# Optimization experiments

Hardware: AMD Instinct MI355X
Metric: run time of the kernel (lower is better)

The kernel has to match this reference:

```python
import jax, jax.numpy as jnp
import numpy as np

N_NODES = 100000
N_EDGES = 600000
DIMS = [128, 64, 32, 2]


def gcn_conv(x, edge_index, W, b, n_nodes):
    """PyG GCNConv (eval mode): symmetric-normalized aggregation with self-loops.
    out = D^{-1/2} (A + I) D^{-1/2} (x W) + b
    """
    h = x @ W  # [N, out] -- transform first (cheaper when out < in)
    src = jnp.concatenate([edge_index[0], jnp.arange(n_nodes)])  # add self-loops
    dst = jnp.concatenate([edge_index[1], jnp.arange(n_nodes)])
    deg = jax.ops.segment_sum(jnp.ones_like(dst, dtype=h.dtype), dst,
                              num_segments=n_nodes)  # in-degree incl. self-loop
    dinv = jax.lax.rsqrt(deg)
    norm = dinv[src] * dinv[dst]  # [E+N]
    msg = norm[:, None] * h[src]  # gather + scale
    out = jax.ops.segment_sum(msg, dst, num_segments=n_nodes)  # scatter-add
    return out + b


def setup_inputs() -> dict:
    key = jax.random.key(0)
    ks = jax.random.split(key, 8)
    x = jax.random.normal(ks[0], (N_NODES, DIMS[0]), dtype=jnp.float32)
    edge_index = jax.random.randint(ks[1], (2, N_EDGES), 0, N_NODES, dtype=jnp.int64)
    inp = {"x": x, "edge_index": edge_index}
    for i in range(3):
        fan_in, fan_out = DIMS[i], DIMS[i + 1]
        s = 1.0 / np.sqrt(fan_in)
        inp[f"W{i+1}"] = jax.random.uniform(ks[2 + 2 * i], (fan_in, fan_out),
                                            minval=-s, maxval=s, dtype=jnp.float32)
        inp[f"b{i+1}"] = jnp.zeros((fan_out,), dtype=jnp.float32)
    return inp


def reference(x, edge_index, W1, b1, W2, b2, W3, b3):
    # 3 stacked GCNConv layers with ReLU; dropout is identity in eval mode.
    n = x.shape[0]
    x = jax.nn.relu(gcn_conv(x, edge_index, W1, b1, n))
    x = jax.nn.relu(gcn_conv(x, edge_index, W2, b2, n))
    x = jax.nn.relu(gcn_conv(x, edge_index, W3, b3, n))
    return x
```

## Files before the change

### kernel.cpp

```cpp
#include <hip/hip_runtime.h>
#include <math.h>


#define FULL_GRID 2048
#define PARTS 8

typedef const __attribute__((address_space(1))) void* gas_ptr;
typedef __attribute__((address_space(3))) void* las_ptr;

__device__ __forceinline__ void gld16(const void* g, void* l) {
  __builtin_amdgcn_global_load_lds((gas_ptr)g, (las_ptr)l, 16, 0, 0);
}

__global__ __launch_bounds__(256) void k_zero(int* __restrict__ p, int n4) {
  int i = blockIdx.x * blockDim.x + threadIdx.x;
  const int stride = gridDim.x * blockDim.x;
  int4* p4 = (int4*)p;
  for (; i < n4; i += stride) p4[i] = make_int4(0, 0, 0, 0);
}

__global__ __launch_bounds__(256) void k_detect(const unsigned int* __restrict__ words,
                                                int* __restrict__ flag) {
  __shared__ int sm[256];
  int cnt = 0;
  #pragma unroll
  for (int j = 0; j < 8; ++j) {
    int idx = (threadIdx.x * 8 + j) * 2 + 1;
    cnt += (words[idx] == 0u) ? 1 : 0;
  }
  sm[threadIdx.x] = cnt;
  __syncthreads();
  for (int off = 128; off > 0; off >>= 1) {
    if (threadIdx.x < off) sm[threadIdx.x] += sm[threadIdx.x + off];
    __syncthreads();
  }
  if (threadIdx.x == 0) flag[0] = (sm[0] > 1024) ? 1 : 0;
}

__global__ __launch_bounds__(256) void k_hist(const void* __restrict__ eraw, int E,
                                              int N, const int* __restrict__ flag,
                                              int* __restrict__ counts) {
  const int is64 = flag[0];
  const int part = blockIdx.x & (PARTS - 1);
  const int lo = (int)((long long)N * part / PARTS);
  const int hi = (int)((long long)N * (part + 1) / PARTS);
  int i = (blockIdx.x >> 3) * blockDim.x + threadIdx.x;
  const int stride = (gridDim.x >> 3) * blockDim.x;
  if (is64) {
    const long long* e = (const long long*)eraw;
    for (; i < E; i += stride) {
      const int d = (int)e[(long long)E + i];
      if (d >= lo && d < hi) atomicAdd(&counts[d], 1);
    }
  } else {
    const int* e = (const int*)eraw;
    for (; i < E; i += stride) {
      const int d = e[E + i];
      if (d >= lo && d < hi) atomicAdd(&counts[d], 1);
    }
  }
}

__global__ __launch_bounds__(1024) void k_scan1(const int* __restrict__ counts,
                                                int* __restrict__ scanned,
                                                int* __restrict__ partials, int n) {
  __shared__ int sm[1024];
  const int i = blockIdx.x * 1024 + threadIdx.x;
  const int v = (i < n) ? counts[i] : 0;
  sm[threadIdx.x] = v;
  __syncthreads();
  for (int off = 1; off < 1024; off <<= 1) {
    int t = sm[threadIdx.x];
    int u = (threadIdx.x >= off) ? sm[threadIdx.x - off] : 0;
    __syncthreads();
    sm[threadIdx.x] = t + u;
    __syncthreads();
  }
  const int inc = sm[threadIdx.x];
  if (i < n) scanned[i] = inc - v;
  if (threadIdx.x == 1023) partials[blockIdx.x] = inc;
}

__global__ __launch_bounds__(1024) void k_scan2(int* __restrict__ partials, int nb) {
  __shared__ int sm[1024];
  const int v = (threadIdx.x < nb) ? partials[threadIdx.x] : 0;
  sm[threadIdx.x] = v;
  __syncthreads();
  for (int off = 1; off < 1024; off <<= 1) {
    int t = sm[threadIdx.x];
    int u = (threadIdx.x >= off) ? sm[threadIdx.x - off] : 0;
    __syncthreads();
    sm[threadIdx.x] = t + u;
    __syncthreads();
  }
  if (threadIdx.x < nb) partials[threadIdx.x] = sm[threadIdx.x] - v;
}

__global__ __launch_bounds__(256) void k_scan3(const int* __restrict__ scanned,
                                               const int* __restrict__ partials,
                                               const int* __restrict__ counts,
                                               int* __restrict__ offsets,
                                               int* __restrict__ cursor,
                                               float* __restrict__ dinv, int n) {
  int i = blockIdx.x * blockDim.x + threadIdx.x;
  const int stride = gridDim.x * blockDim.x;
  for (; i < n; i += stride) {
    const int o = scanned[i] + partials[i >> 10];
    offsets[i] = o;
    cursor[i] = o;
    dinv[i] = rsqrtf((float)counts[i] + 1.0f);
  }
}

__global__ __launch_bounds__(256) void k_fill(const void* __restrict__ eraw, int E,
                                              int N, const int* __restrict__ flag,
                                              int* __restrict__ cursor,
                                              int* __restrict__ elist) {
  const int is64 = flag[0];
  const int part = blockIdx.x & (PARTS - 1);
  const int lo = (int)((long long)N * part / PARTS);
  const int hi = (int)((long long)N * (part + 1) / PARTS);
  int i = (blockIdx.x >> 3) * blockDim.x + threadIdx.x;
  const int stride = (gridDim.x >> 3) * blockDim.x;
  if (is64) {
    const long long* e = (const long long*)eraw;
    for (; i < E; i += stride) {
      const int d = (int)e[(long long)E + i];
      if (d >= lo && d < hi) {
        const int s = (int)e[i];
        elist[atomicAdd(&cursor[d], 1)] = s;
      }
    }
  } else {
    const int* e = (const int*)eraw;
    for (; i < E; i += stride) {
      const int d = e[E + i];
      if (d >= lo && d < hi) {
        const int s = e[i];
        elist[atomicAdd(&cursor[d], 1)] = s;
      }
    }
  }
}

template <int F_IN, int F_OUT, int TILE_M, int KC, int THREADS>
__global__ __launch_bounds__(THREADS) void k_transform(const float* __restrict__ X,
                                                       const float* __restrict__ W,
                                                       const float* __restrict__ dinv,
                                                       float* __restrict__ H, int n) {
  constexpr int COLT = F_OUT / 4;
  constexpr int ROWT = THREADS / COLT;
  constexpr int TM = TILE_M / ROWT;
  constexpr int NKC = F_IN / KC;
  constexpr int K4 = F_IN / 4;
  constexpr int NWB = (NKC > 1) ? 2 : 1;
  static_assert(TM * ROWT == TILE_M && COLT * 4 == F_OUT, "tiling");
  static_assert((TILE_M * F_IN * 4) % 1024 == 0 && (KC * F_OUT * 4) % 1024 == 0, "segs");
  static_assert(K4 >= 8, "swizzle range");
  static_assert(ROWT % 8 == 0, "swizzle invariance across r");

  __shared__ __align__(16) float Xs[TILE_M * F_IN];
  __shared__ __align__(16) float Ws[NWB][KC * F_OUT];

  const int tid = threadIdx.x;
  const int lane = tid & 63;
  const int wid = tid >> 6;
  constexpr int NWAVES = THREADS / 64;
  const long long base = (long long)blockIdx.x * TILE_M;

  const float4* __restrict__ X4 = (const float4*)X;
  if (base + TILE_M <= n) {
    constexpr int SEGS = TILE_M * F_IN * 4 / 1024;
    constexpr int PW = SEGS / NWAVES;
    #pragma unroll
    for (int j = 0; j < PW; ++j) {
      const int seg = wid * PW + j;
      const int slot = seg * 64 + lane;
      const int row = slot / K4;
      const int c = slot % K4;
      const int ksrc = c ^ (row & 7);
      gld16(&X4[(base + row) * K4 + ksrc], &Xs[seg * 256]);
    }
  } else {
    for (int slot = tid; slot < TILE_M * K4; slot += THREADS) {
      const int row = slot / K4;
      const int c = slot % K4;
      float4 v = make_float4(0.f, 0.f, 0.f, 0.f);
      if (base + row < n) v = X4[(base + row) * K4 + (c ^ (row & 7))];
      ((float4*)Xs)[slot] = v;
    }
  }

  constexpr int WSEG = KC * F_OUT * 4 / 1024;
  constexpr int WPW = WSEG / NWAVES;
  static_assert(WPW >= 1, "W seg per wave");
  {
    #pragma unroll
    for (int j = 0; j < WPW; ++j) {
      const int seg = wid * WPW + j;
      gld16(W + seg * 256 + lane * 4, &Ws[0][seg * 256]);
    }
  }

  const int ct = tid % COLT;
  const int rt = tid / COLT;
  const int sw = rt & 7;

  float4 acc[TM];
  #pragma unroll
  for (int r = 0; r < TM; ++r) acc[r] = make_float4(0.f, 0.f, 0.f, 0.f);

  const float4* Xs4 = (const float4*)Xs;

  for (int kc = 0; kc < NKC; ++kc) {
    __syncthreads();
    if (NKC > 1 && kc + 1 < NKC) {
      const float* wb = W + (kc + 1) * KC * F_OUT;
      #pragma unroll
      for (int j = 0; j < WPW; ++j) {
        const int seg = wid * WPW + j;
        gld16(wb + seg * 256 + lane * 4, &Ws[(kc + 1) & (NWB - 1)][seg * 256]);
      }
    }
    const float4* Ws4 = (const float4*)Ws[kc & (NWB - 1)];
    #pragma unroll
    for (int k4 = 0; k4 < KC / 4; ++k4) {
      const int kk = kc * (KC / 4) + k4;
      float4 wv0 = Ws4[(k4 * 4 + 0) * COLT + ct];
      float4 wv1 = Ws4[(k4 * 4 + 1) * COLT + ct];
      float4 wv2 = Ws4[(k4 * 4 + 2) * COLT + ct];
      float4 wv3 = Ws4[(k4 * 4 + 3) * COLT + ct];
      #pragma unroll
      for (int r = 0; r < TM; ++r) {
        const float4 xv = Xs4[(rt + r * ROWT) * K4 + (kk ^ sw)];
        acc[r].x = fmaf(xv.x, wv0.x, acc[r].x);
        acc[r].y = fmaf(xv.x, wv0.y, acc[r].y);
        acc[r].z = fmaf(xv.x, wv0.z, acc[r].z);
        acc[r].w = fmaf(xv.x, wv0.w, acc[r].w);
        acc[r].x = fmaf(xv.y, wv1.x, acc[r].x);
        acc[r].y = fmaf(xv.y, wv1.y, acc[r].y);
        acc[r].z = fmaf(xv.y, wv1.z, acc[r].z);
        acc[r].w = fmaf(xv.y, wv1.w, acc[r].w);
        acc[r].x = fmaf(xv.z, wv2.x, acc[r].x);
        acc[r].y = fmaf(xv.z, wv2.y, acc[r].y);
        acc[r].z = fmaf(xv.z, wv2.z, acc[r].z);
        acc[r].w = fmaf(xv.z, wv2.w, acc[r].w);
        acc[r].x = fmaf(xv.w, wv3.x, acc[r].x);
        acc[r].y = fmaf(xv.w, wv3.y, acc[r].y);
        acc[r].z = fmaf(xv.w, wv3.z, acc[r].z);
        acc[r].w = fmaf(xv.w, wv3.w, acc[r].w);
      }
    }
  }

  #pragma unroll
  for (int r = 0; r < TM; ++r) {
    const long long row = base + rt + r * ROWT;
    if (row < n) {
      const float di = dinv[row];
      float4 v = acc[r];
      v.x *= di; v.y *= di; v.z *= di; v.w *= di;
      *(float4*)&H[row * F_OUT + ct * 4] = v;
    }
  }
}

template <int F, bool RELU_OUT, bool FUSE_W3>
__global__ __launch_bounds__(256) void k_aggregate(const float* __restrict__ HS,
                                                   const float* __restrict__ dinv,
                                                   const int* __restrict__ offsets,
                                                   const int* __restrict__ counts,
                                                   const int* __restrict__ elist,
                                                   const float* __restrict__ bias,
                                                   const float* __restrict__ W3,
                                                   float* __restrict__ out, int n) {
  const int f = threadIdx.x % F;
  const int grp = threadIdx.x / F;
  constexpr int GRPS = 256 / F;
  const float bf = bias[f];
  float w30 = 0.f, w31 = 0.f;
  if (FUSE_W3) { w30 = W3[f * 2 + 0]; w31 = W3[f * 2 + 1]; }

  for (long long d = (long long)blockIdx.x * GRPS + grp; d < n;
       d += (long long)gridDim.x * GRPS) {
    const float di = dinv[d];
    float acc = HS[d * F + f];
    const int start = offsets[d];
    const int cnt = counts[d];
    for (int j = 0; j < cnt; j += 8) {
      int idx[8];
      float v[8];
      #pragma unroll
      for (int t = 0; t < 8; ++t) {
        const int jj = (j + t < cnt) ? (j + t) : j;
        idx[t] = elist[start + jj];
      }
      #pragma unroll
      for (int t = 0; t < 8; ++t) v[t] = HS[(long long)idx[t] * F + f];
      #pragma unroll
      for (int t = 0; t < 8; ++t) acc += (j + t < cnt) ? v[t] : 0.f;
    }

    float r = fmaf(di, acc, bf);
    if (RELU_OUT) r = fmaxf(r, 0.f);
    if (!FUSE_W3) {
      out[d * F + f] = r;
    } else {
      float t0 = r * w30, t1 = r * w31;
      #pragma unroll
      for (int m = 1; m < 32; m <<= 1) {
        t0 += __shfl_xor(t0, m, 64);
        t1 += __shfl_xor(t1, m, 64);
      }
      if (f == 0) {
        out[d * 2 + 0] = di * t0;
        out[d * 2 + 1] = di * t1;
      }
    }
  }
}

extern "C" void kernel_launch(void* const* d_in, const int* in_sizes, int n_in,
                              void* d_out, int out_size, void* d_ws, size_t ws_size,
                              hipStream_t stream) {
  const float* x = (const float*)d_in[0];
  const void* eraw = d_in[1];
  const float* W1 = (const float*)d_in[2];
  const float* b1 = (const float*)d_in[3];
  const float* W2 = (const float*)d_in[4];
  const float* b2 = (const float*)d_in[5];
  const float* W3 = (const float*)d_in[6];
  const float* b3 = (const float*)d_in[7];
  float* out = (float*)d_out;

  const int N = in_sizes[0] / 128;
  const int E = in_sizes[1] / 2;

  char* ws = (char*)d_ws;
  size_t off = 0;
  auto alloc = [&](size_t bytes) -> char* {
    char* p = ws + off;
    off = (off + bytes + 255) & ~(size_t)255;
    return p;
  };
  int*   flag     = (int*)alloc(256);
  int*   counts   = (int*)alloc((size_t)N * 4 + 16);
  int*   scanned  = (int*)alloc((size_t)N * 4);
  int*   partials = (int*)alloc(1024 * 4);
  int*   offsets  = (int*)alloc((size_t)N * 4);
  int*   cursor   = (int*)alloc((size_t)N * 4);
  int*   elist    = (int*)alloc((size_t)E * 4);
  float* dinv     = (float*)alloc((size_t)N * 4);
  float* hbuf     = (float*)alloc((size_t)N * 64 * 4);
  float* obuf     = (float*)alloc((size_t)N * 64 * 4);
  float* h2buf    = (float*)alloc((size_t)N * 32 * 4);
  (void)ws_size; (void)n_in; (void)out_size;

  k_zero<<<128, 256, 0, stream>>>(counts, (N + 3) / 4);
  k_detect<<<1, 256, 0, stream>>>((const unsigned int*)eraw, flag);
  k_hist<<<FULL_GRID, 256, 0, stream>>>(eraw, E, N, flag, counts);
  const int NB = (N + 1023) >> 10;
  k_scan1<<<NB, 1024, 0, stream>>>(counts, scanned, partials, N);
  k_scan2<<<1, 1024, 0, stream>>>(partials, NB);
  k_scan3<<<(N + 255) / 256, 256, 0, stream>>>(scanned, partials, counts, offsets,
                                               cursor, dinv, N);
  k_fill<<<FULL_GRID, 256, 0, stream>>>(eraw, E, N, flag, cursor, elist);

  k_transform<128, 64, 128, 16, 256><<<(N + 127) / 128, 256, 0, stream>>>(
      x, W1, dinv, hbuf, N);
  k_aggregate<64, true, false><<<(N + 3) / 4, 256, 0, stream>>>(
      hbuf, dinv, offsets, counts, elist, b1, nullptr, obuf, N);

  k_transform<64, 32, 128, 64, 256><<<(N + 127) / 128, 256, 0, stream>>>(
      obuf, W2, dinv, h2buf, N);
  k_aggregate<32, true, true><<<(N + 7) / 8, 256, 0, stream>>>(
      h2buf, dinv, offsets, counts, elist, b2, W3, hbuf, N);

  k_aggregate<2, true, false><<<(N + 127) / 128, 256, 0, stream>>>(
      hbuf, dinv, offsets, counts, elist, b3, nullptr, out, N);
}
```

Baseline: 197.1 us.

## Vectorize aggregation per wave, merge init kernels, fold scan2, shrink transform tile

Adds a wave-per-node aggregation kernel in which lanes load float4 slices of several neighbours at once and combine them with cross-lane shuffles, replacing the thread-per-feature gather for layers 1 and 2. It also merges the zero and dtype-detect kernels into one launch and drops the second scan kernel by having every scan3 block redo the small partials scan serially in shared memory. The first transform uses a smaller row tile. These cut launch count and per-edge index-load overhead, in exchange for redundant serial scan work in every block and more shuffle reduction per node.

New measurement: 194.2 us. No clear change (-1.5%).

```diff
diff --git a/kernel.cpp b/kernel.cpp
--- a/kernel.cpp
+++ b/kernel.cpp
@@ -12,29 +12,30 @@
   __builtin_amdgcn_global_load_lds((gas_ptr)g, (las_ptr)l, 16, 0, 0);
 }
 
-__global__ __launch_bounds__(256) void k_zero(int* __restrict__ p, int n4) {
+__global__ __launch_bounds__(256) void k_init(int* __restrict__ p, int n4,
+                                              const unsigned int* __restrict__ words,
+                                              int* __restrict__ flag) {
+  if (blockIdx.x == gridDim.x - 1) {
+    __shared__ int sm[256];
+    int cnt = 0;
+    #pragma unroll
+    for (int j = 0; j < 8; ++j) {
+      int idx = (threadIdx.x * 8 + j) * 2 + 1;
+      cnt += (words[idx] == 0u) ? 1 : 0;
+    }
+    sm[threadIdx.x] = cnt;
+    __syncthreads();
+    for (int off = 128; off > 0; off >>= 1) {
+      if (threadIdx.x < off) sm[threadIdx.x] += sm[threadIdx.x + off];
+      __syncthreads();
+    }
+    if (threadIdx.x == 0) flag[0] = (sm[0] > 1024) ? 1 : 0;
+    return;
+  }
   int i = blockIdx.x * blockDim.x + threadIdx.x;
-  const int stride = gridDim.x * blockDim.x;
+  const int stride = (gridDim.x - 1) * blockDim.x;
   int4* p4 = (int4*)p;
   for (; i < n4; i += stride) p4[i] = make_int4(0, 0, 0, 0);
-}
-
-__global__ __launch_bounds__(256) void k_detect(const unsigned int* __restrict__ words,
-                                                int* __restrict__ flag) {
-  __shared__ int sm[256];
-  int cnt = 0;
-  #pragma unroll
-  for (int j = 0; j < 8; ++j) {
-    int idx = (threadIdx.x * 8 + j) * 2 + 1;
-    cnt += (words[idx] == 0u) ? 1 : 0;
-  }
-  sm[threadIdx.x] = cnt;
-  __syncthreads();
-  for (int off = 128; off > 0; off >>= 1) {
-    if (threadIdx.x < off) sm[threadIdx.x] += sm[threadIdx.x + off];
-    __syncthreads();
-  }
-  if (threadIdx.x == 0) flag[0] = (sm[0] > 1024) ? 1 : 0;
 }
 
 __global__ __launch_bounds__(256) void k_hist(const void* __restrict__ eraw, int E,
@@ -81,31 +82,25 @@
   if (threadIdx.x == 1023) partials[blockIdx.x] = inc;
 }
 
-__global__ __launch_bounds__(1024) void k_scan2(int* __restrict__ partials, int nb) {
-  __shared__ int sm[1024];
-  const int v = (threadIdx.x < nb) ? partials[threadIdx.x] : 0;
-  sm[threadIdx.x] = v;
-  __syncthreads();
-  for (int off = 1; off < 1024; off <<= 1) {
-    int t = sm[threadIdx.x];
-    int u = (threadIdx.x >= off) ? sm[threadIdx.x - off] : 0;
-    __syncthreads();
-    sm[threadIdx.x] = t + u;
-    __syncthreads();
-  }
-  if (threadIdx.x < nb) partials[threadIdx.x] = sm[threadIdx.x] - v;
-}
-
 __global__ __launch_bounds__(256) void k_scan3(const int* __restrict__ scanned,
                                                const int* __restrict__ partials,
+                                               int nb,
                                                const int* __restrict__ counts,
                                                int* __restrict__ offsets,
                                                int* __restrict__ cursor,
                                                float* __restrict__ dinv, int n) {
+  __shared__ int ps[1024];
+  for (int t = threadIdx.x; t < nb; t += 256) ps[t] = partials[t];
+  __syncthreads();
+  if (threadIdx.x == 0) {
+    int run = 0;
+    for (int b = 0; b < nb; ++b) { const int v = ps[b]; ps[b] = run; run += v; }
+  }
+  __syncthreads();
   int i = blockIdx.x * blockDim.x + threadIdx.x;
   const int stride = gridDim.x * blockDim.x;
   for (; i < n; i += stride) {
-    const int o = scanned[i] + partials[i >> 10];
+    const int o = scanned[i] + ps[i >> 10];
     offsets[i] = o;
     cursor[i] = o;
     dinv[i] = rsqrtf((float)counts[i] + 1.0f);
@@ -143,13 +138,13 @@
   }
 }
 
-template <int F_IN, int F_OUT, int TILE_M, int KC, int THREADS>
-__global__ __launch_bounds__(THREADS) void k_transform(const float* __restrict__ X,
-                                                       const float* __restrict__ W,
-                                                       const float* __restrict__ dinv,
-                                                       float* __restrict__ H, int n) {
+template <int F_IN, int F_OUT, int TILE_M, int KC>
+__global__ __launch_bounds__(256) void k_transform(const float* __restrict__ X,
+                                                   const float* __restrict__ W,
+                                                   const float* __restrict__ dinv,
+                                                   float* __restrict__ H, int n) {
   constexpr int COLT = F_OUT / 4;
-  constexpr int ROWT = THREADS / COLT;
+  constexpr int ROWT = 256 / COLT;
   constexpr int TM = TILE_M / ROWT;
   constexpr int NKC = F_IN / KC;
   constexpr int K4 = F_IN / 4;
@@ -165,13 +160,12 @@
   const int tid = threadIdx.x;
   const int lane = tid & 63;
   const int wid = tid >> 6;
-  constexpr int NWAVES = THREADS / 64;
   const long long base = (long long)blockIdx.x * TILE_M;
 
   const float4* __restrict__ X4 = (const float4*)X;
   if (base + TILE_M <= n) {
     constexpr int SEGS = TILE_M * F_IN * 4 / 1024;
-    constexpr int PW = SEGS / NWAVES;
+    constexpr int PW = SEGS / 4;
     #pragma unroll
     for (int j = 0; j < PW; ++j) {
       const int seg = wid * PW + j;
@@ -182,7 +176,7 @@
       gld16(&X4[(base + row) * K4 + ksrc], &Xs[seg * 256]);
     }
   } else {
-    for (int slot = tid; slot < TILE_M * K4; slot += THREADS) {
+    for (int slot = tid; slot < TILE_M * K4; slot += 256) {
       const int row = slot / K4;
       const int c = slot % K4;
       float4 v = make_float4(0.f, 0.f, 0.f, 0.f);
@@ -192,8 +186,7 @@
   }
 
   constexpr int WSEG = KC * F_OUT * 4 / 1024;
-  constexpr int WPW = WSEG / NWAVES;
-  static_assert(WPW >= 1, "W seg per wave");
+  constexpr int WPW = WSEG / 4;
   {
     #pragma unroll
     for (int j = 0; j < WPW; ++j) {
@@ -266,20 +259,99 @@
 }
 
 template <int F, bool RELU_OUT, bool FUSE_W3>
+__global__ __launch_bounds__(256) void k_agg_vec(const float* __restrict__ HS,
+                                                 const float* __restrict__ dinv,
+                                                 const int* __restrict__ offsets,
+                                                 const int* __restrict__ counts,
+                                                 const int* __restrict__ elist,
+                                                 const float* __restrict__ bias,
+                                                 const float* __restrict__ W3,
+                                                 float* __restrict__ out, int n) {
+  constexpr int LPE = F / 4;
+  constexpr int EPW = 64 / LPE;
+  const int lane = threadIdx.x & 63;
+  const int wv = (blockIdx.x * (blockDim.x >> 6)) + (threadIdx.x >> 6);
+  const int nwaves = gridDim.x * (blockDim.x >> 6);
+  const int g = lane / LPE;
+  const int fl = lane % LPE;
+  const float4 bf = *(const float4*)&bias[fl * 4];
+
+  float w3a0 = 0.f, w3a1 = 0.f, w3a2 = 0.f, w3a3 = 0.f;
+  float w3b0 = 0.f, w3b1 = 0.f, w3b2 = 0.f, w3b3 = 0.f;
+  if (FUSE_W3) {
+    w3a0 = W3[(fl * 4 + 0) * 2 + 0]; w3b0 = W3[(fl * 4 + 0) * 2 + 1];
+    w3a1 = W3[(fl * 4 + 1) * 2 + 0]; w3b1 = W3[(fl * 4 + 1) * 2 + 1];
+    w3a2 = W3[(fl * 4 + 2) * 2 + 0]; w3b2 = W3[(fl * 4 + 2) * 2 + 1];
+    w3a3 = W3[(fl * 4 + 3) * 2 + 0]; w3b3 = W3[(fl * 4 + 3) * 2 + 1];
+  }
+
+  for (long long d = wv; d < n; d += nwaves) {
+    const float di = dinv[d];
+    const int start = offsets[d];
+    const int cnt = counts[d];
+    float4 acc = make_float4(0.f, 0.f, 0.f, 0.f);
+    if (g == 0) acc = *(const float4*)&HS[d * F + fl * 4];
+
+    for (int j = 0; j < cnt; j += 2 * EPW) {
+      const int e0 = j + g;
+      const int e1 = j + EPW + g;
+      const int i0 = elist[start + (e0 < cnt ? e0 : cnt - 1)];
+      const int i1 = elist[start + (e1 < cnt ? e1 : cnt - 1)];
+      const float4 v0 = *(const float4*)&HS[(long long)i0 * F + fl * 4];
+      const float4 v1 = *(const float4*)&HS[(long long)i1 * F + fl * 4];
+      if (e0 < cnt) {
+        acc.x += v0.x; acc.y += v0.y; acc.z += v0.z; acc.w += v0.w;
+      }
+      if (e1 < cnt) {
+        acc.x += v1.x; acc.y += v1.y; acc.z += v1.z; acc.w += v1.w;
+      }
+    }
+    #pragma unroll
+    for (int m = LPE; m < 64; m <<= 1) {
+      acc.x += __shfl_xor(acc.x, m, 64);
+      acc.y += __shfl_xor(acc.y, m, 64);
+      acc.z += __shfl_xor(acc.z, m, 64);
+      acc.w += __shfl_xor(acc.w, m, 64);
+    }
+    float4 r;
+    r.x = fmaf(di, acc.x, bf.x);
+    r.y = fmaf(di, acc.y, bf.y);
+    r.z = fmaf(di, acc.z, bf.z);
+    r.w = fmaf(di, acc.w, bf.w);
+    if (RELU_OUT) {
+      r.x = fmaxf(r.x, 0.f); r.y = fmaxf(r.y, 0.f);
+      r.z = fmaxf(r.z, 0.f); r.w = fmaxf(r.w, 0.f);
+    }
+    if (!FUSE_W3) {
+      if (g == 0) *(float4*)&out[d * F + fl * 4] = r;
+    } else {
+      float t0 = r.x * w3a0 + r.y * w3a1 + r.z * w3a2 + r.w * w3a3;
+      float t1 = r.x * w3b0 + r.y * w3b1 + r.z * w3b2 + r.w * w3b3;
+      #pragma unroll
+      for (int m = 1; m < LPE; m <<= 1) {
+        t0 += __shfl_xor(t0, m, 64);
+        t1 += __shfl_xor(t1, m, 64);
+      }
+      if (lane == 0) {
+        out[d * 2 + 0] = di * t0;
+        out[d * 2 + 1] = di * t1;
+      }
+    }
+  }
+}
+
+template <int F, bool RELU_OUT>
 __global__ __launch_bounds__(256) void k_aggregate(const float* __restrict__ HS,
                                                    const float* __restrict__ dinv,
                                                    const int* __restrict__ offsets,
                                                    const int* __restrict__ counts,
                                                    const int* __restrict__ elist,
                                                    const float* __restrict__ bias,
-                                                   const float* __restrict__ W3,
                                                    float* __restrict__ out, int n) {
   const int f = threadIdx.x % F;
   const int grp = threadIdx.x / F;
   constexpr int GRPS = 256 / F;
   const float bf = bias[f];
-  float w30 = 0.f, w31 = 0.f;
-  if (FUSE_W3) { w30 = W3[f * 2 + 0]; w31 = W3[f * 2 + 1]; }
 
   for (long long d = (long long)blockIdx.x * GRPS + grp; d < n;
        d += (long long)gridDim.x * GRPS) {
@@ -300,23 +372,9 @@
       #pragma unroll
       for (int t = 0; t < 8; ++t) acc += (j + t < cnt) ? v[t] : 0.f;
     }
-
     float r = fmaf(di, acc, bf);
     if (RELU_OUT) r = fmaxf(r, 0.f);
-    if (!FUSE_W3) {
-      out[d * F + f] = r;
-    } else {
-      float t0 = r * w30, t1 = r * w31;
-      #pragma unroll
-      for (int m = 1; m < 32; m <<= 1) {
-        t0 += __shfl_xor(t0, m, 64);
-        t1 += __shfl_xor(t1, m, 64);
-      }
-      if (f == 0) {
-        out[d * 2 + 0] = di * t0;
-        out[d * 2 + 1] = di * t1;
-      }
-    }
+    out[d * F + f] = r;
   }
 }
 
@@ -356,26 +414,24 @@
   float* h2buf    = (float*)alloc((size_t)N * 32 * 4);
   (void)ws_size; (void)n_in; (void)out_size;
 
-  k_zero<<<128, 256, 0, stream>>>(counts, (N + 3) / 4);
-  k_detect<<<1, 256, 0, stream>>>((const unsigned int*)eraw, flag);
+  k_init<<<129, 256, 0, stream>>>(counts, (N + 3) / 4, (const unsigned int*)eraw,
+                                  flag);
   k_hist<<<FULL_GRID, 256, 0, stream>>>(eraw, E, N, flag, counts);
   const int NB = (N + 1023) >> 10;
   k_scan1<<<NB, 1024, 0, stream>>>(counts, scanned, partials, N);
-  k_scan2<<<1, 1024, 0, stream>>>(partials, NB);
-  k_scan3<<<(N + 255) / 256, 256, 0, stream>>>(scanned, partials, counts, offsets,
-                                               cursor, dinv, N);
+  k_scan3<<<(N + 255) / 256, 256, 0, stream>>>(scanned, partials, NB, counts,
+                                               offsets, cursor, dinv, N);
   k_fill<<<FULL_GRID, 256, 0, stream>>>(eraw, E, N, flag, cursor, elist);
 
-  k_transform<128, 64, 128, 16, 256><<<(N + 127) / 128, 256, 0, stream>>>(
-      x, W1, dinv, hbuf, N);
-  k_aggregate<64, true, false><<<(N + 3) / 4, 256, 0, stream>>>(
+  k_transform<128, 64, 64, 16><<<(N + 63) / 64, 256, 0, stream>>>(x, W1, dinv, hbuf, N);
+  k_agg_vec<64, true, false><<<FULL_GRID, 256, 0, stream>>>(
       hbuf, dinv, offsets, counts, elist, b1, nullptr, obuf, N);
 
-  k_transform<64, 32, 128, 64, 256><<<(N + 127) / 128, 256, 0, stream>>>(
-      obuf, W2, dinv, h2buf, N);
-  k_aggregate<32, true, true><<<(N + 7) / 8, 256, 0, stream>>>(
+  k_transform<64, 32, 128, 64><<<(N + 127) / 128, 256, 0, stream>>>(obuf, W2, dinv,
+                                                                    h2buf, N);
+  k_agg_vec<32, true, true><<<FULL_GRID, 256, 0, stream>>>(
       h2buf, dinv, offsets, counts, elist, b2, W3, hbuf, N);
 
-  k_aggregate<2, true, false><<<(N + 127) / 128, 256, 0, stream>>>(
-      hbuf, dinv, offsets, counts, elist, b3, nullptr, out, N);
-}
+  k_aggregate<2, true><<<(N + 127) / 128, 256, 0, stream>>>(
+      hbuf, dinv, offsets, counts, elist, b3, out, N);
+}
```
